# Optimization experiments

Hardware: AMD Instinct MI355X
Metric: run time of the kernel (lower is better)

Reference implementation:

```python
import jax, jax.numpy as jnp
from jax import lax
import numpy as np

B, C, H, W, K = 8, 256, 128, 128, 4


def setup_inputs() -> dict:
    key = jax.random.key(0)
    ks = jax.random.split(key, 21)
    s = 0.05
    return {
        'frm_feat': jax.random.normal(ks[0], (B, C, H, W), jnp.float32),
        'other_feat': jax.random.normal(ks[1], (B, C, H, W), jnp.float32),
        'conv3x3_w': jax.random.normal(ks[2], (C, 2 * C, 3, 3), jnp.float32) * (1.0 / np.sqrt(2 * C * 9).astype(np.float32)),
        'conv3x3_b': jax.random.normal(ks[3], (C,), jnp.float32) * s,
        'a1_w': jax.random.normal(ks[4], (C, 2), jnp.float32) * s,
        'a1_b': jax.random.normal(ks[5], (C,), jnp.float32) * s,
        'a2_w': jax.random.normal(ks[6], (C, 2), jnp.float32) * s,
        'a2_b': jax.random.normal(ks[7], (C,), jnp.float32) * s,
        'a3_w': jax.random.normal(ks[8], (C, 2), jnp.float32) * s,
        'a3_b': jax.random.normal(ks[9], (C,), jnp.float32) * s,
        'ug_w': jax.random.normal(ks[10], (K, C), jnp.float32) * (1.0 / np.sqrt(C).astype(np.float32)),
        'ug_b': jax.random.normal(ks[11], (K,), jnp.float32) * s,
        'recon_w': jax.random.normal(ks[12], (C, C), jnp.float32) * (1.0 / np.sqrt(C).astype(np.float32)),
        'recon_b': jax.random.normal(ks[13], (C,), jnp.float32) * s,
        'sp_w': jax.random.normal(ks[14], (), jnp.float32),
        'sp_b': jax.random.normal(ks[15], (), jnp.float32) * s,
        'spa_w': jax.random.normal(ks[16], (C, C), jnp.float32) * (1.0 / np.sqrt(C).astype(np.float32)),
        'spa_b': jax.random.normal(ks[17], (C,), jnp.float32) * s,
        'spm_w': jax.random.normal(ks[18], (C, C), jnp.float32) * (1.0 / np.sqrt(C).astype(np.float32)),
        'spm_b': jax.random.normal(ks[19], (C,), jnp.float32) * s,
        'alpha': jnp.float32(0.5),
    }


def _make_U(mode, aw, ab, ug_w, ug_b):
    # mode: [B, N, M] -> U: [B, N, K] (softmax over rank K)
    avg = jnp.mean(mode, axis=2)           # [B, N]
    mx = jnp.max(mode, axis=2)             # [B, N]
    feat = jnp.stack([avg, mx], axis=1)    # [B, 2, N]
    feat = jnp.einsum('co,bon->bcn', aw, feat) + ab[None, :, None]  # adapter 1x1 conv: [B, C, N]
    logits = jnp.einsum('kc,bcn->bnk', ug_w, feat) + ug_b           # U_gen 1x1 conv: [B, N, K]
    return jax.nn.softmax(logits, axis=-1)


def reference(frm_feat, other_feat, conv3x3_w, conv3x3_b, a1_w, a1_b, a2_w, a2_b,
              a3_w, a3_b, ug_w, ug_b, recon_w, recon_b, sp_w, sp_b,
              spa_w, spa_b, spm_w, spm_b, alpha):
    b, c, h, w = frm_feat.shape
    x = jnp.concatenate([frm_feat, other_feat], axis=1)  # [B, 2C, H, W]
    Fm = lax.conv_general_dilated(x, conv3x3_w, (1, 1), 'SAME',
                                  dimension_numbers=('NCHW', 'OIHW', 'NCHW'))
    Fm = Fm + conv3x3_b[None, :, None, None]
    Fm = jnp.where(Fm >= 0, Fm, 0.01 * Fm)  # LeakyReLU(0.01)

    # Three mode unfoldings (same math as torch permute/reshape chains)
    mode1 = Fm.reshape(b, c, h * w)                     # [B, C, HW]
    mode2 = jnp.transpose(Fm, (0, 3, 1, 2)).reshape(b, w, c * h)  # [B, W, CH]
    mode3 = jnp.transpose(Fm, (0, 2, 1, 3)).reshape(b, h, c * w)  # [B, H, CW]

    U1 = _make_U(mode1, a1_w, a1_b, ug_w, ug_b)  # [B, C, K]
    U2 = _make_U(mode2, a2_w, a2_b, ug_w, ug_b)  # [B, W, K]
    U3 = _make_U(mode3, a3_w, a3_b, ug_w, ug_b)  # [B, H, K]

    # CP outer-product reconstruction summed over rank, already in [B,C,H,W] layout
    cp = jnp.einsum('bck,bwk,bhk->bchw', U1, U2, U3)
    cp = jnp.einsum('oc,bchw->bohw', recon_w, cp) + recon_b[None, :, None, None]

    # spatial attention: sigmoid(1x1 conv on U3 @ U2^T)
    spatial_att = jax.nn.sigmoid(sp_w * jnp.einsum('bhk,bwk->bhw', U3, U2)[:, None] + sp_b)  # [B,1,H,W]

    # spectral attention
    U23 = jnp.concatenate([U2, U3], axis=1)              # [B, W+H, K]
    F_spe = jnp.einsum('bck,bnk->bcn', U1, U23)          # [B, C, W+H]
    g_avg = jnp.mean(F_spe, axis=-1)                     # [B, C]
    g_max = jnp.max(F_spe, axis=-1)                      # [B, C]
    spec = jax.nn.sigmoid(g_avg @ spa_w.T + spa_b + g_max @ spm_w.T + spm_b)
    spec = jax.nn.sigmoid(spec)[:, :, None, None]        # double sigmoid as in source, [B,C,1,1]

    Watt = spec * spatial_att                            # [B, C, H, W]
    fused = alpha * Watt * frm_feat + (1.0 - alpha) * (1.0 - Watt) * other_feat
    return fused, cp
```

## Files before the change

kernel.cpp:

```cpp
#include <hip/hip_runtime.h>
#include <math.h>

#define BB 8
#define CC 256
#define HH 128
#define WW 128
#define CP_OFF 33554432

#define ZB_OFF   0
#define P1S_OFF  256
#define P1M_OFF  262400
#define P2S_OFF  524544
#define P2M_OFF  525568
#define P3S_OFF  526592
#define P3M_OFF  527616
#define U2_OFF   528640
#define U3_OFF   532736
#define V1_OFF   536832
#define SPEC_OFF 545024
#define WS_ZERO_BYTES (528640 * 4)

typedef __attribute__((ext_vector_type(8))) short bf16x8;
typedef __attribute__((ext_vector_type(4))) float f32x4;

static __device__ __forceinline__ unsigned short f2bf(float f) {
    unsigned u = __float_as_uint(f);
    unsigned r = u + 0x7FFFu + ((u >> 16) & 1u);
    return (unsigned short)(r >> 16);
}
static __device__ __forceinline__ unsigned fkey(float f) {
    unsigned u = __float_as_uint(f);
    return (u & 0x80000000u) ? ~u : (u | 0x80000000u);
}
static __device__ __forceinline__ float fkeydec(unsigned k) {
    return __uint_as_float((k & 0x80000000u) ? (k & 0x7FFFFFFFu) : ~k);
}
static __device__ __forceinline__ void gl_lds16(const void* g, void* l) {
    typedef const __attribute__((address_space(1))) unsigned int* gas_t;
    typedef __attribute__((address_space(3))) unsigned int* las_t;
    gas_t gp = (gas_t)(uintptr_t)g;
    las_t lp = (las_t)(unsigned int)(uintptr_t)l;
    __builtin_amdgcn_global_load_lds(gp, lp, 16, 0, 0);
}

__global__ __launch_bounds__(256) void wt_kernel(
    const float* __restrict__ cw, unsigned short* __restrict__ Wt)
{
    const int g = blockIdx.x * 256 + threadIdx.x;
    const int co = g >> 9, ci = g & 511;
    const float* s = cw + (size_t)g * 9;
    #pragma unroll
    for (int t = 0; t < 9; t++)
        Wt[((size_t)t * 256 + co) * 512 + ci] = f2bf(s[t]);
}

__global__ __launch_bounds__(256) void xt_kernel(
    const float* __restrict__ frm, const float* __restrict__ oth,
    unsigned short* __restrict__ Xt)
{
    const int w = threadIdx.x & 127, half = threadIdx.x >> 7;
    const int h = blockIdx.x, b = blockIdx.y;
    const float* src = half ? oth : frm;
    const size_t inbase = (((size_t)b * 256) << 14) + ((size_t)h << 7) + w;
    unsigned short* op = Xt + ((((size_t)(b * 128 + h) * 128) + w) << 9) + half * 256;
    #pragma unroll 2
    for (int c8 = 0; c8 < 32; c8++) {
        unsigned short u[8];
        #pragma unroll
        for (int j = 0; j < 8; j++)
            u[j] = f2bf(src[inbase + (((size_t)(c8 * 8 + j)) << 14)]);
        uint4 pk;
        pk.x = (unsigned)u[0] | ((unsigned)u[1] << 16);
        pk.y = (unsigned)u[2] | ((unsigned)u[3] << 16);
        pk.z = (unsigned)u[4] | ((unsigned)u[5] << 16);
        pk.w = (unsigned)u[6] | ((unsigned)u[7] << 16);
        *(uint4*)(op + c8 * 8) = pk;
    }
}

__global__ __launch_bounds__(256, 2) void conv_mfma(
    const unsigned short* __restrict__ Wt,
    const unsigned short* __restrict__ Xt,
    const float* __restrict__ cb,
    const unsigned short* __restrict__ zb,
    float* __restrict__ p1s, unsigned* __restrict__ p1m,
    float* __restrict__ p2s, unsigned* __restrict__ p2m,
    float* __restrict__ p3s, unsigned* __restrict__ p3m)
{
    __shared__ __align__(16) unsigned short lA[2][1560 * 8];
    __shared__ __align__(16) unsigned short lB[2][552 * 8];

    const int tid = threadIdx.x;
    const int swz = (blockIdx.x & 7) * 256 + (blockIdx.x >> 3);
    const int b = swz >> 8;
    const int h = (swz >> 1) & 127;
    const int cohalf = swz & 1;

    const int lane = tid & 63, wid = tid >> 6;
    const int wm = wid & 1, wn = wid >> 1;
    const int l15 = lane & 15, l4 = lane >> 4;

    const unsigned short* baseA[6];
    int dstA[6];
    #pragma unroll
    for (int i = 0; i < 6; i++) {
        const int ch = i * 4 + wid;
        const int r = ch >> 1, half = ch & 1;
        const int kw = r >> 2, ku = r & 3;
        baseA[i] = Wt + (size_t)(cohalf * 128 + half * 64 + lane) * 512
                      + kw * 131072 + ku * 8;
        dstA[i] = (r * 130 + half * 64) * 8;
    }
    const unsigned short* baseB[3];
    bool okB[3];
    int dstB[3];
    #pragma unroll
    for (int j = 0; j < 3; j++) {
        const int wi = j * 64 + lane;
        const int wg = wi - 1;
        okB[j] = (wg >= 0) && (wg < WW);
        baseB[j] = Xt + (size_t)b * 8388608
                      + (size_t)(okB[j] ? wg : 0) * 512 + wid * 8;
        dstB[j] = (wid * 138 + j * 64) * 8;
    }

    f32x4 acc[4][4];
    #pragma unroll
    for (int m = 0; m < 4; m++)
        #pragma unroll
        for (int n = 0; n < 4; n++)
            acc[m][n] = (f32x4){0.f, 0.f, 0.f, 0.f};

    auto stage = [&](int q, int bufi) {
        const int kh = q >> 4;
        const int ci0 = (q & 15) << 5;
        const int hr = h + kh - 1;
        const bool hv = (hr >= 0) && (hr < HH);
        const int aoff = kh * 393216 + ci0;
        const int boff = (hv ? hr : 0) * 65536 + ci0;
        #pragma unroll
        for (int i = 0; i < 6; i++)
            gl_lds16(baseA[i] + aoff, &lA[bufi][dstA[i]]);
        #pragma unroll
        for (int j = 0; j < 2; j++) {
            const unsigned short* s = (hv && okB[j]) ? (baseB[j] + boff) : zb;
            gl_lds16(s, &lB[bufi][dstB[j]]);
        }
        {
            const unsigned short* s = (hv && okB[2]) ? (baseB[2] + boff) : zb;
            if (lane < 8) gl_lds16(s, &lB[bufi][dstB[2]]);
        }
    };

    auto compute = [&](int cur) {
        const unsigned short* A  = lA[cur];
        const unsigned short* Bl = lB[cur];
        #pragma unroll
        for (int kw = 0; kw < 3; kw++) {
            bf16x8 af[4], bfr[4];
            #pragma unroll
            for (int m = 0; m < 4; m++) {
                const int unit = (kw * 4 + l4) * 130 + wm * 64 + m * 16 + l15;
                af[m] = *(const bf16x8*)&A[unit * 8];
            }
            #pragma unroll
            for (int n = 0; n < 4; n++) {
                const int unit = l4 * 138 + wn * 64 + n * 16 + l15 + kw;
                bfr[n] = *(const bf16x8*)&Bl[unit * 8];
            }
            #pragma unroll
            for (int m = 0; m < 4; m++)
                #pragma unroll
                for (int n = 0; n < 4; n++)
                    acc[m][n] = __builtin_amdgcn_mfma_f32_16x16x32_bf16(
                        af[m], bfr[n], acc[m][n], 0, 0, 0);
        }
    };

    stage(0, 0);

    #pragma unroll 1
    for (int q = 0; q < 47; q++) {
        const int cur = q & 1;
        stage(q + 1, cur ^ 1);
        asm volatile("s_waitcnt vmcnt(9)" ::: "memory");
        __builtin_amdgcn_s_barrier();
        __builtin_amdgcn_sched_barrier(0);
        __builtin_amdgcn_s_setprio(1);
        compute(cur);
        __builtin_amdgcn_s_setprio(0);
        __builtin_amdgcn_sched_barrier(0);
        __builtin_amdgcn_s_barrier();
    }
    asm volatile("s_waitcnt vmcnt(0)" ::: "memory");
    __builtin_amdgcn_s_barrier();
    __builtin_amdgcn_sched_barrier(0);
    __builtin_amdgcn_s_setprio(1);
    compute(1);
    __builtin_amdgcn_s_setprio(0);

    const int cob = cohalf * 128 + wm * 64;
    float t1s[4][4], t1m[4][4], s2[4], x2[4];
    #pragma unroll
    for (int n = 0; n < 4; n++) { s2[n] = 0.f; x2[n] = -INFINITY; }

    #pragma unroll
    for (int m = 0; m < 4; m++) {
        const float4 bb4 = *(const float4*)&cb[cob + m * 16 + l4 * 4];
        float bbv[4] = { bb4.x, bb4.y, bb4.z, bb4.w };
        #pragma unroll
        for (int r = 0; r < 4; r++) { t1s[m][r] = 0.f; t1m[m][r] = -INFINITY; }
        #pragma unroll
        for (int n = 0; n < 4; n++) {
            #pragma unroll
            for (int r = 0; r < 4; r++) {
                float v = acc[m][n][r] + bbv[r];
                v = (v >= 0.f) ? v : 0.01f * v;
                t1s[m][r] += v;
                t1m[m][r] = fmaxf(t1m[m][r], v);
                s2[n] += v;
                x2[n] = fmaxf(x2[n], v);
            }
        }
    }
    #pragma unroll
    for (int m = 0; m < 4; m++)
        #pragma unroll
        for (int r = 0; r < 4; r++) {
            float s = t1s[m][r], x = t1m[m][r];
            #pragma unroll
            for (int off = 1; off <= 8; off <<= 1) {
                s += __shfl_xor(s, off);
                x = fmaxf(x, __shfl_xor(x, off));
            }
            t1s[m][r] = s; t1m[m][r] = x;
        }
    if (l15 == 0) {
        #pragma unroll
        for (int m = 0; m < 4; m++)
            #pragma unroll
            for (int r = 0; r < 4; r++) {
                const int co = cob + m * 16 + l4 * 4 + r;
                const int idx = (b * 256 + co) * 128 + h;
                atomicAdd(&p1s[idx], t1s[m][r]);
                atomicMax(&p1m[idx], fkey(t1m[m][r]));
            }
    }
    float s3 = 0.f, x3 = -INFINITY;
    #pragma unroll
    for (int n = 0; n < 4; n++) {
        float s = s2[n], x = x2[n];
        s += __shfl_xor(s, 16); s += __shfl_xor(s, 32);
        x = fmaxf(x, __shfl_xor(x, 16)); x = fmaxf(x, __shfl_xor(x, 32));
        if (l4 == n) {
            const int w = wn * 64 + n * 16 + l15;
            atomicAdd(&p2s[b * 128 + w], s);
            atomicMax(&p2m[b * 128 + w], fkey(x));
        }
        s3 += s; x3 = fmaxf(x3, x);
    }
    #pragma unroll
    for (int off = 1; off <= 8; off <<= 1) {
        s3 += __shfl_xor(s3, off);
        x3 = fmaxf(x3, __shfl_xor(x3, off));
    }
    if (lane == 0) {
        atomicAdd(&p3s[b * 128 + h], s3);
        atomicMax(&p3m[b * 128 + h], fkey(x3));
    }
}

__device__ inline float blockSum256(float v, float* red)
{
    #pragma unroll
    for (int off = 32; off >= 1; off >>= 1) v += __shfl_xor(v, off);
    const int wave = threadIdx.x >> 6, lane = threadIdx.x & 63;
    __syncthreads();
    if (lane == 0) red[wave] = v;
    __syncthreads();
    return red[0] + red[1] + red[2] + red[3];
}

__device__ inline void softmax4(const float* A, const float* M, const float* Bc,
                                float avg, float mx, float* u)
{
    float l0 = fmaf(A[0], avg, fmaf(M[0], mx, Bc[0]));
    float l1 = fmaf(A[1], avg, fmaf(M[1], mx, Bc[1]));
    float l2 = fmaf(A[2], avg, fmaf(M[2], mx, Bc[2]));
    float l3 = fmaf(A[3], avg, fmaf(M[3], mx, Bc[3]));
    const float mm = fmaxf(fmaxf(l0, l1), fmaxf(l2, l3));
    const float e0 = expf(l0 - mm), e1 = expf(l1 - mm);
    const float e2 = expf(l2 - mm), e3 = expf(l3 - mm);
    const float inv = 1.f / (e0 + e1 + e2 + e3);
    u[0] = e0 * inv; u[1] = e1 * inv; u[2] = e2 * inv; u[3] = e3 * inv;
}

__global__ void make_u_kernel(
    const float* __restrict__ p1s, const unsigned* __restrict__ p1m,
    const float* __restrict__ p2s, const unsigned* __restrict__ p2m,
    const float* __restrict__ p3s, const unsigned* __restrict__ p3m,
    const float* __restrict__ a1w, const float* __restrict__ a1b,
    const float* __restrict__ a2w, const float* __restrict__ a2b,
    const float* __restrict__ a3w, const float* __restrict__ a3b,
    const float* __restrict__ ugw, const float* __restrict__ ugb,
    const float* __restrict__ rw,
    const float* __restrict__ spaw, const float* __restrict__ spab,
    const float* __restrict__ spmw, const float* __restrict__ spmb,
    float* __restrict__ U2g, float* __restrict__ U3g,
    float* __restrict__ V1g, float* __restrict__ specg)
{
    const int b = blockIdx.x, tid = threadIdx.x;

    __shared__ float red[4];
    __shared__ float coefA[3][4], coefM[3][4], coefB[3][4];
    __shared__ float U1s[256][4], U2s[128][4], U3s[128][4];
    __shared__ float gavg[256], gmax[256];

    const float* aws[3]  = { a1w, a2w, a3w };
    const float* abs_[3] = { a1b, a2b, a3b };
    for (int m = 0; m < 3; m++) {
        for (int k = 0; k < 4; k++) {
            const float u = ugw[k * 256 + tid];
            float va = u * aws[m][tid * 2 + 0];
            float vm = u * aws[m][tid * 2 + 1];
            float vb = u * abs_[m][tid];
            va = blockSum256(va, red);
            vm = blockSum256(vm, red);
            vb = blockSum256(vb, red);
            if (tid == 0) {
                coefA[m][k] = va; coefM[m][k] = vm; coefB[m][k] = vb + ugb[k];
            }
        }
    }
    __syncthreads();

    {
        const float* ps = p1s + ((size_t)b * 256 + tid) * 128;
        const unsigned* pm = p1m + ((size_t)b * 256 + tid) * 128;
        float s = 0.f, mx = -INFINITY;
        for (int hh = 0; hh < 128; hh++) {
            s += ps[hh];
            mx = fmaxf(mx, fkeydec(pm[hh]));
        }
        float u[4];
        softmax4(coefA[0], coefM[0], coefB[0], s * (1.f / 16384.f), mx, u);
        U1s[tid][0] = u[0]; U1s[tid][1] = u[1]; U1s[tid][2] = u[2]; U1s[tid][3] = u[3];
    }
    if (tid < 128) {
        const float avg = p2s[b * 128 + tid] * (1.f / 32768.f);
        const float mx  = fkeydec(p2m[b * 128 + tid]);
        float u[4];
        softmax4(coefA[1], coefM[1], coefB[1], avg, mx, u);
        float* g = U2g + ((size_t)b * 128 + tid) * 4;
        for (int k = 0; k < 4; k++) { U2s[tid][k] = u[k]; g[k] = u[k]; }
    } else {
        const int hh = tid - 128;
        const float avg = p3s[b * 128 + hh] * (1.f / 32768.f);
        const float mx  = fkeydec(p3m[b * 128 + hh]);
        float u[4];
        softmax4(coefA[2], coefM[2], coefB[2], avg, mx, u);
        float* g = U3g + ((size_t)b * 128 + hh) * 4;
        for (int k = 0; k < 4; k++) { U3s[hh][k] = u[k]; g[k] = u[k]; }
    }
    __syncthreads();

    {
        float v0 = 0.f, v1 = 0.f, v2 = 0.f, v3 = 0.f;
        const float* rrow = rw + (size_t)tid * 256;
        for (int c2 = 0; c2 < 256; c2++) {
            const float r = rrow[c2];
            v0 = fmaf(r, U1s[c2][0], v0);
            v1 = fmaf(r, U1s[c2][1], v1);
            v2 = fmaf(r, U1s[c2][2], v2);
            v3 = fmaf(r, U1s[c2][3], v3);
        }
        float* vp = V1g + ((size_t)b * 256 + tid) * 4;
        vp[0] = v0; vp[1] = v1; vp[2] = v2; vp[3] = v3;
    }
    {
        const float a0 = U1s[tid][0], a1 = U1s[tid][1];
        const float a2 = U1s[tid][2], a3 = U1s[tid][3];
        float s = 0.f, m = -INFINITY;
        for (int n = 0; n < 256; n++) {
            const float* u23 = (n < 128) ? U2s[n] : U3s[n - 128];
            const float val = a0 * u23[0] + a1 * u23[1] + a2 * u23[2] + a3 * u23[3];
            s += val; m = fmaxf(m, val);
        }
        gavg[tid] = s * (1.f / 256.f);
        gmax[tid] = m;
    }
    __syncthreads();
    {
        float s = spab[tid] + spmb[tid];
        const float* wa = spaw + (size_t)tid * 256;
        const float* wmp = spmw + (size_t)tid * 256;
        for (int c2 = 0; c2 < 256; c2++) {
            s = fmaf(gavg[c2], wa[c2], s);
            s = fmaf(gmax[c2], wmp[c2], s);
        }
        float sg = 1.f / (1.f + expf(-s));
        sg = 1.f / (1.f + expf(-sg));
        specg[b * 256 + tid] = sg;
    }
}

__global__ __launch_bounds__(256) void final_kernel(
    const float* __restrict__ frm, const float* __restrict__ oth,
    const float* __restrict__ U2g, const float* __restrict__ U3g,
    const float* __restrict__ V1g, const float* __restrict__ specg,
    const float* __restrict__ rb,  const float* __restrict__ spw,
    const float* __restrict__ spb, const float* __restrict__ alphap,
    float* __restrict__ out)
{
    const int w  = threadIdx.x & 127;
    const int cc = threadIdx.x >> 7;
    const int h  = blockIdx.x;
    const int c  = blockIdx.y * 2 + cc;
    const int b  = blockIdx.z;

    const float4 u2 = *(const float4*)(U2g + ((size_t)b * 128 + w) * 4);
    const float4 u3 = *(const float4*)(U3g + ((size_t)b * 128 + h) * 4);
    const float4 v1 = *(const float4*)(V1g + ((size_t)b * 256 + c) * 4);

    const float p0 = u2.x * u3.x, p1 = u2.y * u3.y;
    const float p2 = u2.z * u3.z, p3 = u2.w * u3.w;
    const float dot = p0 + p1 + p2 + p3;
    const float att = 1.f / (1.f + expf(-(spw[0] * dot + spb[0])));
    const float cp  = v1.x * p0 + v1.y * p1 + v1.z * p2 + v1.w * p3 + rb[c];

    const float spec  = specg[b * 256 + c];
    const float Watt  = spec * att;
    const float alpha = alphap[0];

    const size_t idx = (((size_t)b * 256 + c) << 14) + ((size_t)h << 7) + w;
    const float f = frm[idx], o = oth[idx];
    out[idx]          = alpha * Watt * f + (1.f - alpha) * (1.f - Watt) * o;
    out[CP_OFF + idx] = cp;
}

extern "C" void kernel_launch(void* const* d_in, const int* in_sizes, int n_in,
                              void* d_out, int out_size, void* d_ws, size_t ws_size,
                              hipStream_t stream)
{
    const float* frm   = (const float*)d_in[0];
    const float* oth   = (const float*)d_in[1];
    const float* cw    = (const float*)d_in[2];
    const float* cb    = (const float*)d_in[3];
    const float* a1w   = (const float*)d_in[4];
    const float* a1b   = (const float*)d_in[5];
    const float* a2w   = (const float*)d_in[6];
    const float* a2b   = (const float*)d_in[7];
    const float* a3w   = (const float*)d_in[8];
    const float* a3b   = (const float*)d_in[9];
    const float* ugw   = (const float*)d_in[10];
    const float* ugb   = (const float*)d_in[11];
    const float* rw    = (const float*)d_in[12];
    const float* rb    = (const float*)d_in[13];
    const float* spw   = (const float*)d_in[14];
    const float* spb   = (const float*)d_in[15];
    const float* spaw  = (const float*)d_in[16];
    const float* spab  = (const float*)d_in[17];
    const float* spmw  = (const float*)d_in[18];
    const float* spmb  = (const float*)d_in[19];
    const float* alpha = (const float*)d_in[20];

    float* out = (float*)d_out;
    float* ws  = (float*)d_ws;

    unsigned short* Wt = (unsigned short*)out;
    unsigned short* Xt = (unsigned short*)(out + CP_OFF);

    float*    zb  = ws + ZB_OFF;
    float*    p1s = ws + P1S_OFF;
    unsigned* p1m = (unsigned*)(ws + P1M_OFF);
    float*    p2s = ws + P2S_OFF;
    unsigned* p2m = (unsigned*)(ws + P2M_OFF);
    float*    p3s = ws + P3S_OFF;
    unsigned* p3m = (unsigned*)(ws + P3M_OFF);
    float*    U2g = ws + U2_OFF;
    float*    U3g = ws + U3_OFF;
    float*    V1g = ws + V1_OFF;
    float*    spc = ws + SPEC_OFF;

    hipMemsetAsync(d_ws, 0, WS_ZERO_BYTES, stream);

    wt_kernel<<<dim3(512), 256, 0, stream>>>(cw, Wt);
    xt_kernel<<<dim3(HH, BB), 256, 0, stream>>>(frm, oth, Xt);

    conv_mfma<<<dim3(2048), 256, 0, stream>>>(
        Wt, Xt, cb, (const unsigned short*)zb,
        p1s, p1m, p2s, p2m, p3s, p3m);

    make_u_kernel<<<dim3(BB), 256, 0, stream>>>(
        p1s, p1m, p2s, p2m, p3s, p3m,
        a1w, a1b, a2w, a2b, a3w, a3b, ugw, ugb,
        rw, spaw, spab, spmw, spmb,
        U2g, U3g, V1g, spc);

    final_kernel<<<dim3(HH, CC / 2, BB), 256, 0, stream>>>(
        frm, oth, U2g, U3g, V1g, spc, rb, spw, spb, alpha, out);
}
```

Baseline: 1.141 ms.

## Pre-swizzle conv weights into MFMA fragment order and load A directly to registers

The weight transpose kernel now writes bf16 weights in an MFMA-fragment-major layout, so each lane can fetch its A operand with contiguous 16-byte global loads. The conv kernel drops the LDS staging buffer for A and double-buffers A fragments in registers alongside the LDS-staged B tiles, with the main loop unrolled by two. The aim is to cut LDS traffic and capacity and avoid redundant LDS reads of weights. In exchange it adds 24 extra VGPRs of bf16x8 per thread, which may limit occupancy or cause spills, and each wave now reads weights from global or L2 without sharing through LDS.

```diff
diff --git a/kernel.cpp b/kernel.cpp
--- a/kernel.cpp
+++ b/kernel.cpp
@@ -44,14 +44,22 @@
 }
 
 __global__ __launch_bounds__(256) void wt_kernel(
-    const float* __restrict__ cw, unsigned short* __restrict__ Wt)
+    const float* __restrict__ cw, unsigned short* __restrict__ WtF)
 {
     const int g = blockIdx.x * 256 + threadIdx.x;
     const int co = g >> 9, ci = g & 511;
+    const int fg = co >> 4, l15c = co & 15;
+    const int cic = ci >> 5, l4c = (ci >> 3) & 3, e = ci & 7;
+    const int lane = l4c * 16 + l15c;
     const float* s = cw + (size_t)g * 9;
     #pragma unroll
-    for (int t = 0; t < 9; t++)
-        Wt[((size_t)t * 256 + co) * 512 + ci] = f2bf(s[t]);
+    for (int kh = 0; kh < 3; kh++)
+        #pragma unroll
+        for (int kw = 0; kw < 3; kw++) {
+            const size_t dst =
+                ((((size_t)(kh * 16 + cic) * 3 + kw) * 16 + fg) * 64 + lane) * 8 + e;
+            WtF[dst] = f2bf(s[kh * 3 + kw]);
+        }
 }
 
 __global__ __launch_bounds__(256) void xt_kernel(
@@ -79,7 +87,7 @@
 }
 
 __global__ __launch_bounds__(256, 2) void conv_mfma(
-    const unsigned short* __restrict__ Wt,
+    const unsigned short* __restrict__ WtF,
     const unsigned short* __restrict__ Xt,
     const float* __restrict__ cb,
     const unsigned short* __restrict__ zb,
@@ -87,8 +95,7 @@
     float* __restrict__ p2s, unsigned* __restrict__ p2m,
     float* __restrict__ p3s, unsigned* __restrict__ p3m)
 {
-    __shared__ __align__(16) unsigned short lA[2][1560 * 8];
-    __shared__ __align__(16) unsigned short lB[2][552 * 8];
+    __shared__ __align__(16) unsigned short lB[2][544 * 8];
 
     const int tid = threadIdx.x;
     const int swz = (blockIdx.x & 7) * 256 + (blockIdx.x >> 3);
@@ -99,18 +106,8 @@
     const int lane = tid & 63, wid = tid >> 6;
     const int wm = wid & 1, wn = wid >> 1;
     const int l15 = lane & 15, l4 = lane >> 4;
-
-    const unsigned short* baseA[6];
-    int dstA[6];
-    #pragma unroll
-    for (int i = 0; i < 6; i++) {
-        const int ch = i * 4 + wid;
-        const int r = ch >> 1, half = ch & 1;
-        const int kw = r >> 2, ku = r & 3;
-        baseA[i] = Wt + (size_t)(cohalf * 128 + half * 64 + lane) * 512
-                      + kw * 131072 + ku * 8;
-        dstA[i] = (r * 130 + half * 64) * 8;
-    }
+    const int fgBase = cohalf * 8 + wm * 4;
+
     const unsigned short* baseB[3];
     bool okB[3];
     int dstB[3];
@@ -121,8 +118,9 @@
         okB[j] = (wg >= 0) && (wg < WW);
         baseB[j] = Xt + (size_t)b * 8388608
                       + (size_t)(okB[j] ? wg : 0) * 512 + wid * 8;
-        dstB[j] = (wid * 138 + j * 64) * 8;
-    }
+        dstB[j] = (wid * 136 + j * 64) * 8;
+    }
+    const unsigned short* baseA = WtF + (size_t)fgBase * 512 + (size_t)lane * 8;
 
     f32x4 acc[4][4];
     #pragma unroll
@@ -131,16 +129,12 @@
         for (int n = 0; n < 4; n++)
             acc[m][n] = (f32x4){0.f, 0.f, 0.f, 0.f};
 
-    auto stage = [&](int q, int bufi) {
+    auto stageB = [&](int q, int bufi) {
         const int kh = q >> 4;
         const int ci0 = (q & 15) << 5;
         const int hr = h + kh - 1;
         const bool hv = (hr >= 0) && (hr < HH);
-        const int aoff = kh * 393216 + ci0;
         const int boff = (hv ? hr : 0) * 65536 + ci0;
-        #pragma unroll
-        for (int i = 0; i < 6; i++)
-            gl_lds16(baseA[i] + aoff, &lA[bufi][dstA[i]]);
         #pragma unroll
         for (int j = 0; j < 2; j++) {
             const unsigned short* s = (hv && okB[j]) ? (baseB[j] + boff) : zb;
@@ -152,20 +146,22 @@
         }
     };
 
-    auto compute = [&](int cur) {
-        const unsigned short* A  = lA[cur];
-        const unsigned short* Bl = lB[cur];
+    auto loadA = [&](int q, bf16x8 (&r)[12]) {
+        const unsigned short* p = baseA + (size_t)q * 24576;
+        #pragma unroll
+        for (int kw = 0; kw < 3; kw++)
+            #pragma unroll
+            for (int m = 0; m < 4; m++)
+                r[kw * 4 + m] = *(const bf16x8*)(p + kw * 8192 + m * 512);
+    };
+
+    auto compute = [&](const unsigned short* Bl, bf16x8 (&rA)[12]) {
         #pragma unroll
         for (int kw = 0; kw < 3; kw++) {
-            bf16x8 af[4], bfr[4];
-            #pragma unroll
-            for (int m = 0; m < 4; m++) {
-                const int unit = (kw * 4 + l4) * 130 + wm * 64 + m * 16 + l15;
-                af[m] = *(const bf16x8*)&A[unit * 8];
-            }
+            bf16x8 bfr[4];
             #pragma unroll
             for (int n = 0; n < 4; n++) {
-                const int unit = l4 * 138 + wn * 64 + n * 16 + l15 + kw;
+                const int unit = l4 * 136 + wn * 64 + n * 16 + l15 + kw;
                 bfr[n] = *(const bf16x8*)&Bl[unit * 8];
             }
             #pragma unroll
@@ -173,30 +169,55 @@
                 #pragma unroll
                 for (int n = 0; n < 4; n++)
                     acc[m][n] = __builtin_amdgcn_mfma_f32_16x16x32_bf16(
-                        af[m], bfr[n], acc[m][n], 0, 0, 0);
+                        rA[kw * 4 + m], bfr[n], acc[m][n], 0, 0, 0);
         }
     };
 
-    stage(0, 0);
+    bf16x8 rA0[12], rA1[12];
+
+    stageB(0, 0);
+    loadA(0, rA0);
 
     #pragma unroll 1
-    for (int q = 0; q < 47; q++) {
-        const int cur = q & 1;
-        stage(q + 1, cur ^ 1);
-        asm volatile("s_waitcnt vmcnt(9)" ::: "memory");
+    for (int q = 0; q < 46; q += 2) {
+        stageB(q + 1, 1);
+        loadA(q + 1, rA1);
+        __builtin_amdgcn_sched_barrier(0);
+        asm volatile("s_waitcnt vmcnt(15)" ::: "memory");
         __builtin_amdgcn_s_barrier();
         __builtin_amdgcn_sched_barrier(0);
         __builtin_amdgcn_s_setprio(1);
-        compute(cur);
+        compute(lB[0], rA0);
         __builtin_amdgcn_s_setprio(0);
         __builtin_amdgcn_sched_barrier(0);
         __builtin_amdgcn_s_barrier();
-    }
-    asm volatile("s_waitcnt vmcnt(0)" ::: "memory");
+
+        stageB(q + 2, 0);
+        loadA(q + 2, rA0);
+        __builtin_amdgcn_sched_barrier(0);
+        asm volatile("s_waitcnt vmcnt(15)" ::: "memory");
+        __builtin_amdgcn_s_barrier();
+        __builtin_amdgcn_sched_barrier(0);
+        __builtin_amdgcn_s_setprio(1);
+        compute(lB[1], rA1);
+        __builtin_amdgcn_s_setprio(0);
+        __builtin_amdgcn_sched_barrier(0);
+        __builtin_amdgcn_s_barrier();
+    }
+    stageB(47, 1);
+    loadA(47, rA1);
+    __builtin_amdgcn_sched_barrier(0);
+    asm volatile("s_waitcnt vmcnt(15)" ::: "memory");
     __builtin_amdgcn_s_barrier();
     __builtin_amdgcn_sched_barrier(0);
     __builtin_amdgcn_s_setprio(1);
-    compute(1);
+    compute(lB[0], rA0);
+    __builtin_amdgcn_s_setprio(0);
+    __builtin_amdgcn_sched_barrier(0);
+    asm volatile("s_waitcnt vmcnt(0)" ::: "memory");
+    __builtin_amdgcn_s_barrier();
+    __builtin_amdgcn_s_setprio(1);
+    compute(lB[1], rA1);
     __builtin_amdgcn_s_setprio(0);
 
     const int cob = cohalf * 128 + wm * 64;
```

After: 1.018 ms. -10.8%, faster.
